# Performance work log

Measured on AMD Instinct MI355X. Metric: run time of the kernel, lower is better.

## Reference

```python
import jax, jax.numpy as jnp
import numpy as np

N = 262144          # total nodes
D = 256             # feature dim
D_OUT = 128
NUM_SEGMENTS = 4096 # number of graphs/sets


def setup_inputs() -> dict:
    key = jax.random.key(0)
    ks = jax.random.split(key, 8)
    sc = 1.0 / np.sqrt(D)
    x = jax.random.normal(ks[0], (N, D), dtype=jnp.float32)
    index = jnp.sort(jax.random.randint(ks[1], (N,), 0, NUM_SEGMENTS)).astype(jnp.int32)
    W1 = jax.random.normal(ks[2], (D, D), dtype=jnp.float32) * sc
    b1 = jnp.zeros((D,), dtype=jnp.float32)
    W2 = jax.random.normal(ks[3], (D, D), dtype=jnp.float32) * sc
    b2 = jnp.zeros((D,), dtype=jnp.float32)
    W3 = jax.random.normal(ks[4], (D, D), dtype=jnp.float32) * sc
    b3 = jnp.zeros((D,), dtype=jnp.float32)
    W4 = jax.random.normal(ks[5], (D, D_OUT), dtype=jnp.float32) * sc
    b4 = jnp.zeros((D_OUT,), dtype=jnp.float32)
    return {"x": x, "index": index, "W1": W1, "b1": b1, "W2": W2, "b2": b2,
            "W3": W3, "b3": b3, "W4": W4, "b4": b4}


def reference(x, index, W1, b1, W2, b2, W3, b3, W4, b4):
    # score_net: 2-layer SiLU MLP, per node -> scores s [N, D]
    s = jax.nn.silu(x @ W1 + b1) @ W2 + b2
    # scatter_softmax over nodes grouped by segment index (dim=0)
    m = jax.ops.segment_max(s, index, num_segments=NUM_SEGMENTS)  # [B, D]
    e = jnp.exp(s - jax.lax.stop_gradient(m)[index])              # [N, D]
    denom = jax.ops.segment_sum(e, index, num_segments=NUM_SEGMENTS)  # [B, D]
    attn = e / denom[index]                                       # [N, D]
    # weighted segment sum: sum_splits(s * x, splits)
    sx = jax.ops.segment_sum(attn * x, index, num_segments=NUM_SEGMENTS)  # [B, D]
    # readout_net: 2-layer SiLU MLP per segment
    out = jax.nn.silu(sx @ W3 + b3) @ W4 + b4                     # [B, D_OUT]
    return out
```

## Files before the change

### kernel.cpp

```cpp
#include <hip/hip_runtime.h>

typedef _Float16 half8 __attribute__((ext_vector_type(8)));
typedef float f32x4 __attribute__((ext_vector_type(4)));

#define LDS_AS __attribute__((address_space(3)))
#define GLB_AS __attribute__((address_space(1)))

__device__ __forceinline__ void load_lds16(const void* g, void* l) {
    __builtin_amdgcn_global_load_lds((const GLB_AS unsigned int*)g,
                                     (LDS_AS unsigned int*)l, 16, 0, 0);
}

#define CHUNK 65536
#define TILES_PER_CHUNK 2048
#define GRID1 512

__global__ void prep_weights(const float* __restrict__ W1, const float* __restrict__ W2,
                             const float* __restrict__ W3, const float* __restrict__ W4,
                             _Float16* __restrict__ W1t, _Float16* __restrict__ W2t,
                             _Float16* __restrict__ W3t, _Float16* __restrict__ W4t) {
    int e = blockIdx.x * 256 + threadIdx.x;
    if (e < 196608) {
        int sel = e >> 16, r = e & 65535;
        const float* src = sel == 0 ? W1 : (sel == 1 ? W2 : W3);
        _Float16* dst = sel == 0 ? W1t : (sel == 1 ? W2t : W3t);
        int n = r >> 8, k = r & 255;
        dst[n * 256 + k] = (_Float16)src[k * 256 + n];
    } else {
        int r = e - 196608;
        int n = r >> 8, k = r & 255;
        W4t[n * 256 + k] = (_Float16)W4[k * 128 + n];
    }
}

__global__ __launch_bounds__(256, 2)
void gemm1(const float* __restrict__ x, const _Float16* __restrict__ W1t,
           const float* __restrict__ b1, _Float16* __restrict__ hh, int row_base)
{
    __shared__ __align__(16) float Abuf[2][32 * 256];

    const int tid = threadIdx.x;
    const int w = tid >> 6, lane = tid & 63;
    const int q = lane >> 4, l15 = lane & 15;

    half8 Bf[4][8];
#pragma unroll
    for (int j = 0; j < 4; ++j)
#pragma unroll
        for (int kc = 0; kc < 8; ++kc)
            Bf[j][kc] = *(const half8*)(W1t + (size_t)(w * 64 + j * 16 + l15) * 256 + kc * 32 + q * 8);

    float b1v[4];
#pragma unroll
    for (int j = 0; j < 4; ++j) b1v[j] = b1[w * 64 + j * 16 + l15];

    auto stage = [&](int b, int t) {
        const float* src = x + (size_t)(row_base + t * 32) * 256;
#pragma unroll
        for (int p = 0; p < 8; ++p) {
            int c = p * 256 + tid;
            int r = c >> 6, pc = c & 63;
            int lc = pc ^ (r & 7);
            load_lds16(src + (size_t)r * 256 + lc * 4, &Abuf[b][c * 4]);
        }
    };

    int cur = 0;
    stage(0, (int)blockIdx.x);
#pragma unroll 1
    for (int t = blockIdx.x; t < TILES_PER_CHUNK; t += GRID1) {
        __syncthreads();
        if (t + GRID1 < TILES_PER_CHUNK) stage(cur ^ 1, t + GRID1);

        const float* Ab = Abuf[cur];
        f32x4 acc[2][4];
#pragma unroll
        for (int i = 0; i < 2; ++i)
#pragma unroll
            for (int j = 0; j < 4; ++j) acc[i][j] = (f32x4){0.f, 0.f, 0.f, 0.f};

#pragma unroll
        for (int kc = 0; kc < 8; ++kc) {
            half8 af[2];
#pragma unroll
            for (int i = 0; i < 2; ++i) {
                int row = i * 16 + l15;
                int s = row & 7;
                f32x4 lo = *(const f32x4*)(Ab + row * 256 + (((kc * 8 + q * 2) ^ s) * 4));
                f32x4 hi = *(const f32x4*)(Ab + row * 256 + (((kc * 8 + q * 2 + 1) ^ s) * 4));
#pragma unroll
                for (int c = 0; c < 4; ++c) { af[i][c] = (_Float16)lo[c]; af[i][4 + c] = (_Float16)hi[c]; }
            }
#pragma unroll
            for (int i = 0; i < 2; ++i)
#pragma unroll
                for (int j = 0; j < 4; ++j)
                    acc[i][j] = __builtin_amdgcn_mfma_f32_16x16x32_f16(af[i], Bf[j][kc], acc[i][j], 0, 0, 0);
        }

        const int grow0 = t * 32;
#pragma unroll
        for (int i = 0; i < 2; ++i)
#pragma unroll
            for (int j = 0; j < 4; ++j)
#pragma unroll
                for (int r = 0; r < 4; ++r) {
                    float v = acc[i][j][r] + b1v[j];
                    float sv = v / (1.f + __expf(-v));
                    hh[(size_t)(grow0 + i * 16 + q * 4 + r) * 256 + w * 64 + j * 16 + l15] = (_Float16)sv;
                }
        cur ^= 1;
    }
}

__global__ __launch_bounds__(256, 2)
void gemm2(const _Float16* __restrict__ hh, const _Float16* __restrict__ W2t,
           const float* __restrict__ b2, const float* __restrict__ x,
           const int* __restrict__ index, float* __restrict__ gnum,
           float* __restrict__ gden, int row_base)
{
    __shared__ __align__(16) _Float16 Abuf[2][32 * 256];
    __shared__ __align__(16) float etile[32 * 257];
    __shared__ int sl[32];

    const int tid = threadIdx.x;
    const int w = tid >> 6, lane = tid & 63;
    const int q = lane >> 4, l15 = lane & 15;

    half8 Bf[4][8];
#pragma unroll
    for (int j = 0; j < 4; ++j)
#pragma unroll
        for (int kc = 0; kc < 8; ++kc)
            Bf[j][kc] = *(const half8*)(W2t + (size_t)(w * 64 + j * 16 + l15) * 256 + kc * 32 + q * 8);

    float b2v[4];
#pragma unroll
    for (int j = 0; j < 4; ++j) b2v[j] = b2[w * 64 + j * 16 + l15];

    auto stage = [&](int b, int t) {
        const _Float16* src = hh + (size_t)(t * 32) * 256;
#pragma unroll
        for (int p = 0; p < 4; ++p) {
            int c = p * 256 + tid;
            int r = c >> 5, pc = c & 31;
            int lc = pc ^ (r & 7);
            load_lds16(src + (size_t)r * 256 + lc * 8, &Abuf[b][c * 8]);
        }
    };

    int cur = 0;
    stage(0, (int)blockIdx.x);
#pragma unroll 1
    for (int t = blockIdx.x; t < TILES_PER_CHUNK; t += GRID1) {
        __syncthreads();
        if (t + GRID1 < TILES_PER_CHUNK) stage(cur ^ 1, t + GRID1);
        if (tid < 32) sl[tid] = index[row_base + t * 32 + tid];

        const _Float16* Ab = Abuf[cur];
        f32x4 acc[2][4];
#pragma unroll
        for (int i = 0; i < 2; ++i)
#pragma unroll
            for (int j = 0; j < 4; ++j) acc[i][j] = (f32x4){0.f, 0.f, 0.f, 0.f};

#pragma unroll
        for (int kc = 0; kc < 8; ++kc) {
            half8 af[2];
#pragma unroll
            for (int i = 0; i < 2; ++i) {
                int row = i * 16 + l15;
                af[i] = *(const half8*)(Ab + row * 256 + (((kc * 4 + q) ^ (row & 7)) * 8));
            }
#pragma unroll
            for (int i = 0; i < 2; ++i)
#pragma unroll
                for (int j = 0; j < 4; ++j)
                    acc[i][j] = __builtin_amdgcn_mfma_f32_16x16x32_f16(af[i], Bf[j][kc], acc[i][j], 0, 0, 0);
        }

#pragma unroll
        for (int i = 0; i < 2; ++i)
#pragma unroll
            for (int j = 0; j < 4; ++j)
#pragma unroll
                for (int r = 0; r < 4; ++r)
                    etile[(i * 16 + q * 4 + r) * 257 + w * 64 + j * 16 + l15] =
                        __expf(acc[i][j][r] + b2v[j]);
        __syncthreads();

        {
            const float* gx = x + (size_t)(row_base + t * 32) * 256 + tid;
            float aN = 0.f, aD = 0.f;
            int curseg = sl[0];
#pragma unroll 1
            for (int hb = 0; hb < 2; ++hb) {
                float xv[16];
#pragma unroll
                for (int r = 0; r < 16; ++r) xv[r] = gx[(size_t)(hb * 16 + r) * 256];
#pragma unroll
                for (int r = 0; r < 16; ++r) {
                    int rr = hb * 16 + r;
                    int sg = sl[rr];
                    if (sg != curseg) {
                        atomicAdd(&gnum[(size_t)curseg * 256 + tid], aN);
                        atomicAdd(&gden[(size_t)curseg * 256 + tid], aD);
                        aN = 0.f; aD = 0.f; curseg = sg;
                    }
                    float e = etile[rr * 257 + tid];
                    aN += e * xv[r];
                    aD += e;
                }
            }
            atomicAdd(&gnum[(size_t)curseg * 256 + tid], aN);
            atomicAdd(&gden[(size_t)curseg * 256 + tid], aD);
        }
        cur ^= 1;
    }
}

__global__ void normalize_sx(const float* __restrict__ num, const float* __restrict__ den,
                             _Float16* __restrict__ sx) {
    int i = blockIdx.x * 256 + threadIdx.x;
    float d = den[i];
    sx[i] = (_Float16)((d > 0.f) ? num[i] / d : 0.f);
}

__global__ __launch_bounds__(256, 2)
void readout1(const _Float16* __restrict__ sx, const _Float16* __restrict__ W3t,
              const float* __restrict__ b3, _Float16* __restrict__ h2)
{
    __shared__ __align__(16) _Float16 Ah[64 * 256];
    const int tid = threadIdx.x;
    const int w = tid >> 6, lane = tid & 63;
    const int q = lane >> 4, l15 = lane & 15;
    const int row0 = blockIdx.x * 64;

    half8 Bf[4][8];
#pragma unroll
    for (int j = 0; j < 4; ++j)
#pragma unroll
        for (int kc = 0; kc < 8; ++kc)
            Bf[j][kc] = *(const half8*)(W3t + (size_t)(w * 64 + j * 16 + l15) * 256 + kc * 32 + q * 8);
    float bv[4];
#pragma unroll
    for (int j = 0; j < 4; ++j) bv[j] = b3[w * 64 + j * 16 + l15];

#pragma unroll
    for (int p = 0; p < 8; ++p) {
        int c = p * 256 + tid;
        int r = c >> 5, pc = c & 31;
        int lc = pc ^ (r & 7);
        load_lds16(sx + (size_t)(row0 + r) * 256 + lc * 8, &Ah[c * 8]);
    }
    __syncthreads();

    f32x4 acc[4][4];
#pragma unroll
    for (int i = 0; i < 4; ++i)
#pragma unroll
        for (int j = 0; j < 4; ++j) acc[i][j] = (f32x4){0.f, 0.f, 0.f, 0.f};

#pragma unroll
    for (int kc = 0; kc < 8; ++kc) {
        half8 af[4];
#pragma unroll
        for (int i = 0; i < 4; ++i) {
            int row = i * 16 + l15;
            af[i] = *(const half8*)(Ah + row * 256 + (((kc * 4 + q) ^ (row & 7)) * 8));
        }
#pragma unroll
        for (int i = 0; i < 4; ++i)
#pragma unroll
            for (int j = 0; j < 4; ++j)
                acc[i][j] = __builtin_amdgcn_mfma_f32_16x16x32_f16(af[i], Bf[j][kc], acc[i][j], 0, 0, 0);
    }
#pragma unroll
    for (int i = 0; i < 4; ++i)
#pragma unroll
        for (int j = 0; j < 4; ++j)
#pragma unroll
            for (int r = 0; r < 4; ++r) {
                float v = acc[i][j][r] + bv[j];
                float sv = v / (1.f + __expf(-v));
                h2[(size_t)(row0 + i * 16 + q * 4 + r) * 256 + w * 64 + j * 16 + l15] = (_Float16)sv;
            }
}

__global__ __launch_bounds__(256, 2)
void readout2(const _Float16* __restrict__ h2, const _Float16* __restrict__ W4t,
              const float* __restrict__ b4, float* __restrict__ out)
{
    __shared__ __align__(16) _Float16 Ah[64 * 256];
    const int tid = threadIdx.x;
    const int w = tid >> 6, lane = tid & 63;
    const int q = lane >> 4, l15 = lane & 15;
    const int row0 = blockIdx.x * 64;

    half8 Bf[2][8];
#pragma unroll
    for (int j = 0; j < 2; ++j)
#pragma unroll
        for (int kc = 0; kc < 8; ++kc)
            Bf[j][kc] = *(const half8*)(W4t + (size_t)(w * 32 + j * 16 + l15) * 256 + kc * 32 + q * 8);
    float bv[2];
#pragma unroll
    for (int j = 0; j < 2; ++j) bv[j] = b4[w * 32 + j * 16 + l15];

#pragma unroll
    for (int p = 0; p < 8; ++p) {
        int c = p * 256 + tid;
        int r = c >> 5, pc = c & 31;
        int lc = pc ^ (r & 7);
        load_lds16(h2 + (size_t)(row0 + r) * 256 + lc * 8, &Ah[c * 8]);
    }
    __syncthreads();

    f32x4 acc[4][2];
#pragma unroll
    for (int i = 0; i < 4; ++i)
#pragma unroll
        for (int j = 0; j < 2; ++j) acc[i][j] = (f32x4){0.f, 0.f, 0.f, 0.f};

#pragma unroll
    for (int kc = 0; kc < 8; ++kc) {
        half8 af[4];
#pragma unroll
        for (int i = 0; i < 4; ++i) {
            int row = i * 16 + l15;
            af[i] = *(const half8*)(Ah + row * 256 + (((kc * 4 + q) ^ (row & 7)) * 8));
        }
#pragma unroll
        for (int i = 0; i < 4; ++i)
#pragma unroll
            for (int j = 0; j < 2; ++j)
                acc[i][j] = __builtin_amdgcn_mfma_f32_16x16x32_f16(af[i], Bf[j][kc], acc[i][j], 0, 0, 0);
    }
#pragma unroll
    for (int i = 0; i < 4; ++i)
#pragma unroll
        for (int j = 0; j < 2; ++j)
#pragma unroll
            for (int r = 0; r < 4; ++r)
                out[(size_t)(row0 + i * 16 + q * 4 + r) * 128 + w * 32 + j * 16 + l15] =
                    acc[i][j][r] + bv[j];
}

extern "C" void kernel_launch(void* const* d_in, const int* in_sizes, int n_in,
                              void* d_out, int out_size, void* d_ws, size_t ws_size,
                              hipStream_t stream) {
    const float* x   = (const float*)d_in[0];
    const int*   idx = (const int*)d_in[1];
    const float* W1  = (const float*)d_in[2];
    const float* b1  = (const float*)d_in[3];
    const float* W2  = (const float*)d_in[4];
    const float* b2  = (const float*)d_in[5];
    const float* W3  = (const float*)d_in[6];
    const float* b3  = (const float*)d_in[7];
    const float* W4  = (const float*)d_in[8];
    const float* b4  = (const float*)d_in[9];
    char* ws = (char*)d_ws;

    _Float16* hh   = (_Float16*)ws;
    float*    gnum = (float*)(ws + 33554432);
    float*    gden = (float*)(ws + 37748736);
    _Float16* sx   = (_Float16*)(ws + 41943040);
    _Float16* h2   = (_Float16*)(ws + 44040192);
    _Float16* W1t  = (_Float16*)(ws + 46137344);
    _Float16* W2t  = (_Float16*)(ws + 46268416);
    _Float16* W3t  = (_Float16*)(ws + 46399488);
    _Float16* W4t  = (_Float16*)(ws + 46530560);

    prep_weights<<<896, 256, 0, stream>>>(W1, W2, W3, W4, W1t, W2t, W3t, W4t);
    hipMemsetAsync(gnum, 0, 8388608, stream);

    for (int c = 0; c < 4; ++c) {
        gemm1<<<GRID1, 256, 0, stream>>>(x, W1t, b1, hh, c * CHUNK);
        gemm2<<<GRID1, 256, 0, stream>>>(hh, W2t, b2, x, idx, gnum, gden, c * CHUNK);
    }
    normalize_sx<<<4096, 256, 0, stream>>>(gnum, gden, sx);
    readout1<<<64, 256, 0, stream>>>(sx, W3t, b3, h2);
    readout2<<<64, 256, 0, stream>>>(h2, W4t, b4, (float*)d_out);
}
```

Baseline: 555.9 us.

## Fuse both score-MLP GEMMs and segment accumulation into one kernel

Merges gemm1 and gemm2 into a single 512-thread kernel. The SiLU hidden activations stay in swizzled LDS instead of going through a global fp16 buffer, and x is reused from the staged LDS tile rather than reloaded from global. Each block now walks 32 contiguous tiles and carries its segment accumulators across tiles, so atomics are issued only at segment boundaries. This also removes the 4-chunk launch loop. In exchange, the grid is only 256 blocks of 512 threads with larger LDS use, so occupancy and load balance may suffer.

Result: faster. 476.4 us (-14.3%).

```diff
diff --git a/kernel.cpp b/kernel.cpp
--- a/kernel.cpp
+++ b/kernel.cpp
@@ -11,9 +11,8 @@
                                      (LDS_AS unsigned int*)l, 16, 0, 0);
 }
 
-#define CHUNK 65536
-#define TILES_PER_CHUNK 2048
-#define GRID1 512
+#define GRIDF 256
+#define TPB   32
 
 __global__ void prep_weights(const float* __restrict__ W1, const float* __restrict__ W2,
                              const float* __restrict__ W3, const float* __restrict__ W4,
@@ -33,51 +32,68 @@
     }
 }
 
-__global__ __launch_bounds__(256, 2)
-void gemm1(const float* __restrict__ x, const _Float16* __restrict__ W1t,
-           const float* __restrict__ b1, _Float16* __restrict__ hh, int row_base)
+__global__ __launch_bounds__(512, 2)
+void fused(const float* __restrict__ x, const _Float16* __restrict__ W1t,
+           const float* __restrict__ b1, const _Float16* __restrict__ W2t,
+           const float* __restrict__ b2, const int* __restrict__ index,
+           float* __restrict__ gnum, float* __restrict__ gden)
 {
     __shared__ __align__(16) float Abuf[2][32 * 256];
+    __shared__ __align__(16) _Float16 Hh[32 * 256];
+    __shared__ __align__(16) float etile[32 * 257];
+    __shared__ int sl[32];
 
     const int tid = threadIdx.x;
     const int w = tid >> 6, lane = tid & 63;
     const int q = lane >> 4, l15 = lane & 15;
 
-    half8 Bf[4][8];
-#pragma unroll
-    for (int j = 0; j < 4; ++j)
-#pragma unroll
-        for (int kc = 0; kc < 8; ++kc)
-            Bf[j][kc] = *(const half8*)(W1t + (size_t)(w * 64 + j * 16 + l15) * 256 + kc * 32 + q * 8);
-
-    float b1v[4];
-#pragma unroll
-    for (int j = 0; j < 4; ++j) b1v[j] = b1[w * 64 + j * 16 + l15];
+    half8 Bf1[2][8], Bf2[2][8];
+#pragma unroll
+    for (int j = 0; j < 2; ++j)
+#pragma unroll
+        for (int kc = 0; kc < 8; ++kc) {
+            Bf1[j][kc] = *(const half8*)(W1t + (size_t)(w * 32 + j * 16 + l15) * 256 + kc * 32 + q * 8);
+            Bf2[j][kc] = *(const half8*)(W2t + (size_t)(w * 32 + j * 16 + l15) * 256 + kc * 32 + q * 8);
+        }
+    float b1v[2], b2v[2];
+#pragma unroll
+    for (int j = 0; j < 2; ++j) {
+        b1v[j] = b1[w * 32 + j * 16 + l15];
+        b2v[j] = b2[w * 32 + j * 16 + l15];
+    }
+
+    const int t0 = blockIdx.x * TPB;
 
     auto stage = [&](int b, int t) {
-        const float* src = x + (size_t)(row_base + t * 32) * 256;
-#pragma unroll
-        for (int p = 0; p < 8; ++p) {
-            int c = p * 256 + tid;
+        const float* src = x + (size_t)t * 32 * 256;
+#pragma unroll
+        for (int p = 0; p < 4; ++p) {
+            int c = p * 512 + tid;
             int r = c >> 6, pc = c & 63;
             int lc = pc ^ (r & 7);
             load_lds16(src + (size_t)r * 256 + lc * 4, &Abuf[b][c * 4]);
         }
     };
 
+    float aN = 0.f, aD = 0.f;
+    int curseg = -1;
+
     int cur = 0;
-    stage(0, (int)blockIdx.x);
+    stage(0, t0);
 #pragma unroll 1
-    for (int t = blockIdx.x; t < TILES_PER_CHUNK; t += GRID1) {
+    for (int ti = 0; ti < TPB; ++ti) {
+        const int t = t0 + ti;
         __syncthreads();
-        if (t + GRID1 < TILES_PER_CHUNK) stage(cur ^ 1, t + GRID1);
+        if (tid < 32) sl[tid] = index[t * 32 + tid];
+        if (ti + 1 < TPB) stage(cur ^ 1, t + 1);
 
         const float* Ab = Abuf[cur];
-        f32x4 acc[2][4];
+
+        f32x4 acc[2][2];
 #pragma unroll
         for (int i = 0; i < 2; ++i)
 #pragma unroll
-            for (int j = 0; j < 4; ++j) acc[i][j] = (f32x4){0.f, 0.f, 0.f, 0.f};
+            for (int j = 0; j < 2; ++j) acc[i][j] = (f32x4){0.f, 0.f, 0.f, 0.f};
 
 #pragma unroll
         for (int kc = 0; kc < 8; ++kc) {
@@ -94,75 +110,30 @@
 #pragma unroll
             for (int i = 0; i < 2; ++i)
 #pragma unroll
-                for (int j = 0; j < 4; ++j)
-                    acc[i][j] = __builtin_amdgcn_mfma_f32_16x16x32_f16(af[i], Bf[j][kc], acc[i][j], 0, 0, 0);
-        }
-
-        const int grow0 = t * 32;
+                for (int j = 0; j < 2; ++j)
+                    acc[i][j] = __builtin_amdgcn_mfma_f32_16x16x32_f16(af[i], Bf1[j][kc], acc[i][j], 0, 0, 0);
+        }
+
 #pragma unroll
         for (int i = 0; i < 2; ++i)
 #pragma unroll
-            for (int j = 0; j < 4; ++j)
+            for (int j = 0; j < 2; ++j)
 #pragma unroll
                 for (int r = 0; r < 4; ++r) {
                     float v = acc[i][j][r] + b1v[j];
                     float sv = v / (1.f + __expf(-v));
-                    hh[(size_t)(grow0 + i * 16 + q * 4 + r) * 256 + w * 64 + j * 16 + l15] = (_Float16)sv;
+                    int row = i * 16 + q * 4 + r;
+                    int col = w * 32 + j * 16 + l15;
+                    int unit = (col >> 3) ^ (row & 7);
+                    Hh[row * 256 + unit * 8 + (col & 7)] = (_Float16)sv;
                 }
-        cur ^= 1;
-    }
-}
-
-__global__ __launch_bounds__(256, 2)
-void gemm2(const _Float16* __restrict__ hh, const _Float16* __restrict__ W2t,
-           const float* __restrict__ b2, const float* __restrict__ x,
-           const int* __restrict__ index, float* __restrict__ gnum,
-           float* __restrict__ gden, int row_base)
-{
-    __shared__ __align__(16) _Float16 Abuf[2][32 * 256];
-    __shared__ __align__(16) float etile[32 * 257];
-    __shared__ int sl[32];
-
-    const int tid = threadIdx.x;
-    const int w = tid >> 6, lane = tid & 63;
-    const int q = lane >> 4, l15 = lane & 15;
-
-    half8 Bf[4][8];
-#pragma unroll
-    for (int j = 0; j < 4; ++j)
-#pragma unroll
-        for (int kc = 0; kc < 8; ++kc)
-            Bf[j][kc] = *(const half8*)(W2t + (size_t)(w * 64 + j * 16 + l15) * 256 + kc * 32 + q * 8);
-
-    float b2v[4];
-#pragma unroll
-    for (int j = 0; j < 4; ++j) b2v[j] = b2[w * 64 + j * 16 + l15];
-
-    auto stage = [&](int b, int t) {
-        const _Float16* src = hh + (size_t)(t * 32) * 256;
-#pragma unroll
-        for (int p = 0; p < 4; ++p) {
-            int c = p * 256 + tid;
-            int r = c >> 5, pc = c & 31;
-            int lc = pc ^ (r & 7);
-            load_lds16(src + (size_t)r * 256 + lc * 8, &Abuf[b][c * 8]);
-        }
-    };
-
-    int cur = 0;
-    stage(0, (int)blockIdx.x);
-#pragma unroll 1
-    for (int t = blockIdx.x; t < TILES_PER_CHUNK; t += GRID1) {
         __syncthreads();
-        if (t + GRID1 < TILES_PER_CHUNK) stage(cur ^ 1, t + GRID1);
-        if (tid < 32) sl[tid] = index[row_base + t * 32 + tid];
-
-        const _Float16* Ab = Abuf[cur];
-        f32x4 acc[2][4];
+
+        f32x4 acc2[2][2];
 #pragma unroll
         for (int i = 0; i < 2; ++i)
 #pragma unroll
-            for (int j = 0; j < 4; ++j) acc[i][j] = (f32x4){0.f, 0.f, 0.f, 0.f};
+            for (int j = 0; j < 2; ++j) acc2[i][j] = (f32x4){0.f, 0.f, 0.f, 0.f};
 
 #pragma unroll
         for (int kc = 0; kc < 8; ++kc) {
@@ -170,52 +141,57 @@
 #pragma unroll
             for (int i = 0; i < 2; ++i) {
                 int row = i * 16 + l15;
-                af[i] = *(const half8*)(Ab + row * 256 + (((kc * 4 + q) ^ (row & 7)) * 8));
+                af[i] = *(const half8*)(Hh + row * 256 + (((kc * 4 + q) ^ (row & 7)) * 8));
             }
 #pragma unroll
             for (int i = 0; i < 2; ++i)
 #pragma unroll
-                for (int j = 0; j < 4; ++j)
-                    acc[i][j] = __builtin_amdgcn_mfma_f32_16x16x32_f16(af[i], Bf[j][kc], acc[i][j], 0, 0, 0);
+                for (int j = 0; j < 2; ++j)
+                    acc2[i][j] = __builtin_amdgcn_mfma_f32_16x16x32_f16(af[i], Bf2[j][kc], acc2[i][j], 0, 0, 0);
         }
 
 #pragma unroll
         for (int i = 0; i < 2; ++i)
 #pragma unroll
-            for (int j = 0; j < 4; ++j)
+            for (int j = 0; j < 2; ++j)
 #pragma unroll
                 for (int r = 0; r < 4; ++r)
-                    etile[(i * 16 + q * 4 + r) * 257 + w * 64 + j * 16 + l15] =
-                        __expf(acc[i][j][r] + b2v[j]);
+                    etile[(i * 16 + q * 4 + r) * 257 + w * 32 + j * 16 + l15] =
+                        __expf(acc2[i][j][r] + b2v[j]);
         __syncthreads();
 
-        {
-            const float* gx = x + (size_t)(row_base + t * 32) * 256 + tid;
-            float aN = 0.f, aD = 0.f;
-            int curseg = sl[0];
+        if (tid < 256) {
+            const int col = tid;
 #pragma unroll 1
             for (int hb = 0; hb < 2; ++hb) {
                 float xv[16];
 #pragma unroll
-                for (int r = 0; r < 16; ++r) xv[r] = gx[(size_t)(hb * 16 + r) * 256];
+                for (int r = 0; r < 16; ++r) {
+                    int rr = hb * 16 + r;
+                    xv[r] = Ab[rr * 256 + ((((col >> 2) ^ (rr & 7)) << 2) | (col & 3))];
+                }
 #pragma unroll
                 for (int r = 0; r < 16; ++r) {
                     int rr = hb * 16 + r;
                     int sg = sl[rr];
                     if (sg != curseg) {
-                        atomicAdd(&gnum[(size_t)curseg * 256 + tid], aN);
-                        atomicAdd(&gden[(size_t)curseg * 256 + tid], aD);
+                        if (curseg >= 0) {
+                            atomicAdd(&gnum[(size_t)curseg * 256 + col], aN);
+                            atomicAdd(&gden[(size_t)curseg * 256 + col], aD);
+                        }
                         aN = 0.f; aD = 0.f; curseg = sg;
                     }
-                    float e = etile[rr * 257 + tid];
+                    float e = etile[rr * 257 + col];
                     aN += e * xv[r];
                     aD += e;
                 }
             }
-            atomicAdd(&gnum[(size_t)curseg * 256 + tid], aN);
-            atomicAdd(&gden[(size_t)curseg * 256 + tid], aD);
         }
         cur ^= 1;
+    }
+    if (tid < 256 && curseg >= 0) {
+        atomicAdd(&gnum[(size_t)curseg * 256 + tid], aN);
+        atomicAdd(&gden[(size_t)curseg * 256 + tid], aD);
     }
 }
 
@@ -361,23 +337,20 @@
     const float* b4  = (const float*)d_in[9];
     char* ws = (char*)d_ws;
 
-    _Float16* hh   = (_Float16*)ws;
-    float*    gnum = (float*)(ws + 33554432);
-    float*    gden = (float*)(ws + 37748736);
-    _Float16* sx   = (_Float16*)(ws + 41943040);
-    _Float16* h2   = (_Float16*)(ws + 44040192);
-    _Float16* W1t  = (_Float16*)(ws + 46137344);
-    _Float16* W2t  = (_Float16*)(ws + 46268416);
-    _Float16* W3t  = (_Float16*)(ws + 46399488);
-    _Float16* W4t  = (_Float16*)(ws + 46530560);
+    float*    gnum = (float*)ws;
+    float*    gden = (float*)(ws + 4194304);
+    _Float16* sx   = (_Float16*)(ws + 8388608);
+    _Float16* h2   = (_Float16*)(ws + 10485760);
+    _Float16* W1t  = (_Float16*)(ws + 12582912);
+    _Float16* W2t  = (_Float16*)(ws + 12713984);
+    _Float16* W3t  = (_Float16*)(ws + 12845056);
+    _Float16* W4t  = (_Float16*)(ws + 12976128);
 
     prep_weights<<<896, 256, 0, stream>>>(W1, W2, W3, W4, W1t, W2t, W3t, W4t);
-    hipMemsetAsync(gnum, 0, 8388608, stream);
-
-    for (int c = 0; c < 4; ++c) {
-        gemm1<<<GRID1, 256, 0, stream>>>(x, W1t, b1, hh, c * CHUNK);
-        gemm2<<<GRID1, 256, 0, stream>>>(hh, W2t, b2, x, idx, gnum, gden, c * CHUNK);
-    }
+    hipMemsetAsync(ws, 0, 8388608, stream);
+
+    fused<<<GRIDF, 512, 0, stream>>>(x, W1t, b1, W2t, b2, idx, gnum, gden);
+
     normalize_sx<<<4096, 256, 0, stream>>>(gnum, gden, sx);
     readout1<<<64, 256, 0, stream>>>(sx, W3t, b3, h2);
     readout2<<<64, 256, 0, stream>>>(h2, W4t, b4, (float*)d_out);
```
